# Kernel tuning notes

Hardware: AMD Instinct MI355X
Metric: run time of the kernel (lower is better)

Reference implementation:

```python
import jax, jax.numpy as jnp
import numpy as np


def _conv1x1(x, W, b):
    # 1x1 conv == per-pixel channel matmul: x [B,C,H,W], W [O,C], b [O]
    return jnp.einsum('bchw,oc->bohw', x, W) + b[None, :, None, None]


def setup_inputs() -> dict:
    key = jax.random.key(0)
    ks = jax.random.split(key, 9)
    B, C, H, W = 16, 512, 32, 32
    s = 1.0 / np.sqrt(C)
    inp = {
        'x': jax.random.normal(ks[0], (B, C, H, W), dtype=jnp.float32),
        'Wq': jax.random.normal(ks[1], (C, C), dtype=jnp.float32) * s,
        'bq': jax.random.normal(ks[2], (C,), dtype=jnp.float32) * 0.01,
        'Wk': jax.random.normal(ks[3], (C, C), dtype=jnp.float32) * s,
        'bk': jax.random.normal(ks[4], (C,), dtype=jnp.float32) * 0.01,
        'Wv': jax.random.normal(ks[5], (C, C), dtype=jnp.float32) * s,
        'bv': jax.random.normal(ks[6], (C,), dtype=jnp.float32) * 0.01,
        'Wo': jax.random.normal(ks[7], (C, C), dtype=jnp.float32) * s,
        'bo': jax.random.normal(ks[8], (C,), dtype=jnp.float32) * 0.01,
    }
    return inp


def reference(x, Wq, bq, Wk, bk, Wv, bv, Wo, bo):
    B, C, H, W = x.shape
    q = _conv1x1(x, Wq, bq)
    k = _conv1x1(x, Wk, bk)
    v = _conv1x1(x, Wv, bv)
    hw = H * W
    qf = q.reshape(B, C, hw)  # [B,C,HW]
    kf = k.reshape(B, C, hw)
    vf = v.reshape(B, C, hw)
    # scores[b,i,j] = sum_c q[b,c,i] * k[b,c,j], scaled by c^-0.5
    scores = jnp.einsum('bci,bcj->bij', qf, kf) * (C ** -0.5)
    attn = jax.nn.softmax(scores, axis=2)  # softmax over keys j
    # out[b,c,i] = sum_j v[b,c,j] * attn[b,i,j]
    out = jnp.einsum('bcj,bij->bci', vf, attn).reshape(B, C, H, W)
    out = _conv1x1(out, Wo, bo)
    return x + out
```

## Files before the change

kernel.cpp:

```cpp
#include <hip/hip_runtime.h>
#include <hip/hip_bf16.h>
#include <math.h>


typedef __bf16 bf16x8 __attribute__((ext_vector_type(8)));
typedef float  f32x16 __attribute__((ext_vector_type(16)));

__device__ __forceinline__ unsigned short f2bf(float f) {
    unsigned u = __float_as_uint(f);
    u += 0x7fff + ((u >> 16) & 1);
    return (unsigned short)(u >> 16);
}

__device__ __forceinline__ void gload_lds16(const void* g, void* l) {
    __builtin_amdgcn_global_load_lds(
        (const __attribute__((address_space(1))) void*)g,
        (__attribute__((address_space(3))) void*)l, 16, 0, 0);
}

struct GemmP {
    const unsigned short* A;
    const unsigned short* B;
    void* C;
    const float* bias;
    const float* resid;
    float* lsum;
    int M, N, K, ldA, ldB;
    long sA, sB, sC, sR;
    int ln_nn, ln_pb;
    float scale;
};

template<bool OUT_F32, int BIAS_MODE, bool RESID, int EXPM>
__device__ __forceinline__ void gemm_body(const GemmP p, int L,
                                          unsigned short* Als,
                                          unsigned short* Bls)
{
    const int xcd = L & 7;
    const int idx = L >> 3;
    const int bz  = xcd * 2 + (idx >> p.ln_pb);
    const int w   = idx & ((1 << p.ln_pb) - 1);
    const int m0  = (w >> p.ln_nn) << 7;
    const int n0  = (w & ((1 << p.ln_nn) - 1)) << 7;

    const unsigned short* A = p.A + bz * p.sA;
    const unsigned short* B = p.B + bz * p.sB;

    const int tid  = threadIdx.x;
    const int lane = tid & 63;
    const int wave = tid >> 6;
    const int wm   = wave >> 1;
    const int wn   = wave & 1;

    const int ar = lane >> 2;
    const int ak = (((lane & 3) ^ ((ar >> 1) & 3))) * 8;

    const unsigned short* agp = A + (long)(m0 + wave * 16 + ar) * p.ldA + ak;
    const unsigned short* bgp = B + (long)(n0 + wave * 16 + ar) * p.ldB + ak;
    const long aj = 64L * p.ldA;
    const long bj = 64L * p.ldB;

    unsigned short* alw  = Als + wave * 512;
    unsigned short* alwh = Als + (wave + 4) * 512;
    unsigned short* blw  = Bls + wave * 512;
    unsigned short* blwh = Bls + (wave + 4) * 512;

    const int ln31 = lane & 31;
    const int hi   = lane >> 5;
    const int swz  = ((ln31 >> 1) & 3) << 3;
    const int aoff = (wm * 64 + ln31) * 32;
    const int boff = (wn * 64 + ln31) * 32;
    const int koff0 = (hi * 8) ^ swz;
    const int koff1 = (16 + hi * 8) ^ swz;

    f32x16 acc[2][2] = {};

    const int nsteps = p.K >> 5;

    auto STAGE = [&](int sel) {
        gload_lds16(agp,      alw  + sel * 4096);
        gload_lds16(agp + aj, alwh + sel * 4096);
        gload_lds16(bgp,      blw  + sel * 4096);
        gload_lds16(bgp + bj, blwh + sel * 4096);
        agp += 32; bgp += 32;
    };

    auto COMPUTE = [&](int sel) {
        const unsigned short* Ap = Als + sel * 4096;
        const unsigned short* Bp = Bls + sel * 4096;
        bf16x8 af[2][2], bfr[2][2];
        #pragma unroll
        for (int mt = 0; mt < 2; ++mt) {
            af[mt][0] = *(const bf16x8*)&Ap[aoff + mt * 1024 + koff0];
            af[mt][1] = *(const bf16x8*)&Ap[aoff + mt * 1024 + koff1];
        }
        #pragma unroll
        for (int nt = 0; nt < 2; ++nt) {
            bfr[nt][0] = *(const bf16x8*)&Bp[boff + nt * 1024 + koff0];
            bfr[nt][1] = *(const bf16x8*)&Bp[boff + nt * 1024 + koff1];
        }
        #pragma unroll
        for (int ks = 0; ks < 2; ++ks)
            #pragma unroll
            for (int mt = 0; mt < 2; ++mt)
                #pragma unroll
                for (int nt = 0; nt < 2; ++nt)
                    acc[mt][nt] = __builtin_amdgcn_mfma_f32_32x32x16_bf16(
                        af[mt][ks], bfr[nt][ks], acc[mt][nt], 0, 0, 0);
    };

    STAGE(0);
    __syncthreads();

    for (int t = 0; t < nsteps; t += 2) {
        STAGE(1);
        COMPUTE(0);
        __syncthreads();
        if (t + 2 < nsteps) STAGE(0);
        COMPUTE(1);
        __syncthreads();
    }

    float* Cf = (float*)p.C + bz * p.sC;
    unsigned short* Ch = (unsigned short*)p.C + bz * p.sC;
    const float* resid = RESID ? (p.resid + bz * p.sR) : nullptr;
    const int N = p.N;

    if (EXPM == 1) {
        float* lrow = p.lsum + bz * (long)p.M;
        #pragma unroll
        for (int mt = 0; mt < 2; ++mt) {
            #pragma unroll
            for (int r = 0; r < 16; ++r) {
                const int row = m0 + wm * 64 + mt * 32 +
                                (r & 3) + 8 * (r >> 2) + 4 * hi;
                float rs = 0.0f;
                #pragma unroll
                for (int nt = 0; nt < 2; ++nt) {
                    const int col = n0 + wn * 64 + nt * 32 + ln31;
                    const float e = __expf(acc[mt][nt][r] * p.scale);
                    rs += e;
                    Ch[(long)row * N + col] = f2bf(e);
                }
                rs += __shfl_xor(rs, 1);
                rs += __shfl_xor(rs, 2);
                rs += __shfl_xor(rs, 4);
                rs += __shfl_xor(rs, 8);
                rs += __shfl_xor(rs, 16);
                if (ln31 == 0) atomicAdd(&lrow[row], rs);
            }
        }
    } else {
        #pragma unroll
        for (int mt = 0; mt < 2; ++mt) {
            float linv[16];
            if (EXPM == 2) {
                const float* lrow = p.lsum + bz * (long)p.M;
                #pragma unroll
                for (int r = 0; r < 16; ++r)
                    linv[r] = 1.0f / lrow[m0 + wm * 64 + mt * 32 +
                                          (r & 3) + 8 * (r >> 2) + 4 * hi];
            }
            #pragma unroll
            for (int nt = 0; nt < 2; ++nt) {
                const int col = n0 + wn * 64 + nt * 32 + ln31;
                const float bn = (BIAS_MODE == 2) ? p.bias[col] : 0.0f;
                #pragma unroll
                for (int r = 0; r < 16; ++r) {
                    const int row = m0 + wm * 64 + mt * 32 +
                                    (r & 3) + 8 * (r >> 2) + 4 * hi;
                    float val = acc[mt][nt][r] + bn;
                    if (BIAS_MODE == 1) val += p.bias[row];
                    if (EXPM == 2) val *= linv[r];
                    const long o = (long)row * N + col;
                    if (RESID) val += resid[o];
                    if (OUT_F32) Cf[o] = val;
                    else         Ch[o] = f2bf(val);
                }
            }
        }
    }
}

template<bool OUT_F32, int BIAS_MODE, bool RESID, int EXPM>
__global__ __launch_bounds__(256) void gemm_bt_mfma(GemmP p)
{
    __shared__ unsigned short Als[2 * 4096];
    __shared__ unsigned short Bls[2 * 4096];
    gemm_body<OUT_F32, BIAS_MODE, RESID, EXPM>(p, blockIdx.x, Als, Bls);
}

__global__ __launch_bounds__(256) void gemm_qkv_fused(GemmP pqk, GemmP pv, int split)
{
    __shared__ unsigned short Als[2 * 4096];
    __shared__ unsigned short Bls[2 * 4096];
    if ((int)blockIdx.x < split)
        gemm_body<false, 2, false, 0>(pqk, blockIdx.x, Als, Bls);
    else
        gemm_body<false, 1, false, 0>(pv, blockIdx.x - split, Als, Bls);
}

__global__ __launch_bounds__(256) void prep_all(
    const float* __restrict__ x, unsigned short* __restrict__ xT,
    const float* __restrict__ Wq, const float* __restrict__ Wk,
    const float* __restrict__ Wv, const float* __restrict__ Wo,
    const float* __restrict__ bq, const float* __restrict__ bk,
    unsigned short* __restrict__ Wb, float* __restrict__ biasqk,
    float* __restrict__ lsum)
{
    const int b = blockIdx.x;
    const int t = threadIdx.x;
    if (b < 8192) {
        __shared__ float tl[32][33];
        const int batch = b >> 9;
        const int rem = b & 511;
        const int p0 = (rem & 31) * 32;
        const int c0 = (rem >> 5) * 32;
        const float* xb = x + (long)batch * 524288;
        unsigned short* xTb = xT + (long)batch * 524288;
        const int tx = t & 31;
        const int ty = t >> 5;
        #pragma unroll
        for (int i = 0; i < 4; ++i)
            tl[ty + 8 * i][tx] = xb[(long)(c0 + ty + 8 * i) * 1024 + p0 + tx];
        __syncthreads();
        #pragma unroll
        for (int i = 0; i < 4; ++i)
            xTb[(long)(p0 + ty + 8 * i) * 512 + c0 + tx] = f2bf(tl[tx][ty + 8 * i]);
    } else if (b < 9216) {
        const int wb = b - 8192;
        const float* srcs[4] = {Wq, Wk, Wv, Wo};
        const float* s = srcs[wb >> 8];
        unsigned short* d = Wb + (long)(wb >> 8) * 262144;
        const int i = ((wb & 255) * 256 + t) * 4;
        const float4 f = *(const float4*)(s + i);
        ushort4 h;
        h.x = f2bf(f.x); h.y = f2bf(f.y); h.z = f2bf(f.z); h.w = f2bf(f.w);
        *(ushort4*)(d + i) = h;
    } else {
        biasqk[t]       = bq[t];
        biasqk[256 + t] = bq[256 + t];
        biasqk[512 + t] = bk[t];
        biasqk[768 + t] = bk[256 + t];
        #pragma unroll
        for (int i = 0; i < 64; ++i) lsum[i * 256 + t] = 0.0f;
    }
}

extern "C" void kernel_launch(void* const* d_in, const int* in_sizes, int n_in,
                              void* d_out, int out_size, void* d_ws, size_t ws_size,
                              hipStream_t stream)
{
    const float* x  = (const float*)d_in[0];
    const float* Wq = (const float*)d_in[1];
    const float* bq = (const float*)d_in[2];
    const float* Wk = (const float*)d_in[3];
    const float* bk = (const float*)d_in[4];
    const float* Wv = (const float*)d_in[5];
    const float* bv = (const float*)d_in[6];
    const float* Wo = (const float*)d_in[7];
    const float* bo = (const float*)d_in[8];
    float* out = (float*)d_out;

    const int Bn = 16, C = 512, HW = 1024;
    const long CHW = (long)C * HW;
    const long SHW = (long)HW * HW;

    unsigned short* xT   = (unsigned short*)d_ws;
    unsigned short* qkT  = xT + Bn * CHW;
    unsigned short* vB   = qkT + Bn * SHW;
    unsigned short* expS = vB + Bn * CHW;
    unsigned short* Wb   = expS + Bn * SHW;
    float* biasqk = (float*)(Wb + 4 * 262144);
    float* lsum   = biasqk + 1024;
    unsigned short* OT = xT;

    unsigned short* Wvb = Wb + 2 * 262144;
    unsigned short* Wob = Wb + 3 * 262144;

    const dim3 blk(256);
    const float scale = 0.044194173824159216f;

    prep_all<<<dim3(9217), blk, 0, stream>>>(x, xT, Wq, Wk, Wv, Wo, bq, bk,
                                             Wb, biasqk, lsum);

    GemmP pqk = { xT, Wb, qkT, biasqk, nullptr, nullptr,
                  HW, 2 * C, C, C, C, CHW, 0, SHW, 0, 3, 6, 0.0f };
    GemmP pv  = { Wvb, xT, vB, bv, nullptr, nullptr,
                  C, HW, C, C, C, 0, CHW, CHW, 0, 3, 5, 0.0f };
    gemm_qkv_fused<<<dim3(1536), blk, 0, stream>>>(pqk, pv, 1024);

    GemmP ps  = { qkT, qkT + C, expS, nullptr, nullptr, lsum,
                  HW, HW, C, 2 * C, 2 * C, SHW, SHW, SHW, 0, 3, 6, scale };
    gemm_bt_mfma<false, 0, false, 1><<<dim3(1024), blk, 0, stream>>>(ps);

    GemmP po  = { expS, vB, OT, nullptr, nullptr, lsum,
                  HW, C, HW, HW, HW, SHW, CHW, CHW, 0, 2, 5, 0.0f };
    gemm_bt_mfma<false, 0, false, 2><<<dim3(512), blk, 0, stream>>>(po);

    GemmP pout = { Wob, OT, out, bo, x, nullptr,
                   C, HW, C, C, C, 0, CHW, CHW, CHW, 3, 5, 0.0f };
    gemm_bt_mfma<true, 1, true, 0><<<dim3(512), blk, 0, stream>>>(pout);
}
```

Before: 241.3 us.

## Switch GEMM mainloop to triple-buffered LDS pipeline with one barrier per step

Replaces the double-buffered K loop, which has two __syncthreads per pair of steps, with a three-stage LDS ring. Each step has one barrier gated by a partial vmcnt wait, so two global-to-LDS loads stay in flight while the MFMAs run on the current buffer. The aim is to hide global load latency and halve barrier count. LDS use per block goes from 32 KB to 48 KB, which may lower occupancy, and the explicit waitcnt/sched_barrier sequencing is fragile.

```diff
diff --git a/kernel.cpp b/kernel.cpp
--- a/kernel.cpp
+++ b/kernel.cpp
@@ -60,11 +60,6 @@
     const long aj = 64L * p.ldA;
     const long bj = 64L * p.ldB;
 
-    unsigned short* alw  = Als + wave * 512;
-    unsigned short* alwh = Als + (wave + 4) * 512;
-    unsigned short* blw  = Bls + wave * 512;
-    unsigned short* blwh = Bls + (wave + 4) * 512;
-
     const int ln31 = lane & 31;
     const int hi   = lane >> 5;
     const int swz  = ((ln31 >> 1) & 3) << 3;
@@ -78,10 +73,12 @@
     const int nsteps = p.K >> 5;
 
     auto STAGE = [&](int sel) {
-        gload_lds16(agp,      alw  + sel * 4096);
-        gload_lds16(agp + aj, alwh + sel * 4096);
-        gload_lds16(bgp,      blw  + sel * 4096);
-        gload_lds16(bgp + bj, blwh + sel * 4096);
+        unsigned short* a0 = Als + sel * 4096;
+        unsigned short* b0 = Bls + sel * 4096;
+        gload_lds16(agp,      a0 + wave * 512);
+        gload_lds16(agp + aj, a0 + (wave + 4) * 512);
+        gload_lds16(bgp,      b0 + wave * 512);
+        gload_lds16(bgp + bj, b0 + (wave + 4) * 512);
         agp += 32; bgp += 32;
     };
 
@@ -110,16 +107,25 @@
     };
 
     STAGE(0);
-    __syncthreads();
-
-    for (int t = 0; t < nsteps; t += 2) {
-        STAGE(1);
-        COMPUTE(0);
-        __syncthreads();
-        if (t + 2 < nsteps) STAGE(0);
-        COMPUTE(1);
-        __syncthreads();
+    STAGE(1);
+
+    int bc = 0, bn = 1, bs = 2;
+    for (int t = 0; t < nsteps - 1; ++t) {
+        __builtin_amdgcn_sched_barrier(0);
+        asm volatile("s_waitcnt vmcnt(4)" ::: "memory");
+        __builtin_amdgcn_s_barrier();
+        asm volatile("" ::: "memory");
+        __builtin_amdgcn_sched_barrier(0);
+        if (t + 2 < nsteps) STAGE(bs);
+        COMPUTE(bc);
+        const int tmp = bc; bc = bn; bn = bs; bs = tmp;
     }
+    __builtin_amdgcn_sched_barrier(0);
+    asm volatile("s_waitcnt vmcnt(0)" ::: "memory");
+    __builtin_amdgcn_s_barrier();
+    asm volatile("" ::: "memory");
+    __builtin_amdgcn_sched_barrier(0);
+    COMPUTE(bc);
 
     float* Cf = (float*)p.C + bz * p.sC;
     unsigned short* Ch = (unsigned short*)p.C + bz * p.sC;
@@ -164,12 +170,12 @@
             #pragma unroll
             for (int nt = 0; nt < 2; ++nt) {
                 const int col = n0 + wn * 64 + nt * 32 + ln31;
-                const float bn = (BIAS_MODE == 2) ? p.bias[col] : 0.0f;
+                const float bn2 = (BIAS_MODE == 2) ? p.bias[col] : 0.0f;
                 #pragma unroll
                 for (int r = 0; r < 16; ++r) {
                     const int row = m0 + wm * 64 + mt * 32 +
                                     (r & 3) + 8 * (r >> 2) + 4 * hi;
-                    float val = acc[mt][nt][r] + bn;
+                    float val = acc[mt][nt][r] + bn2;
                     if (BIAS_MODE == 1) val += p.bias[row];
                     if (EXPM == 2) val *= linv[r];
                     const long o = (long)row * N + col;
@@ -185,15 +191,15 @@
 template<bool OUT_F32, int BIAS_MODE, bool RESID, int EXPM>
 __global__ __launch_bounds__(256) void gemm_bt_mfma(GemmP p)
 {
-    __shared__ unsigned short Als[2 * 4096];
-    __shared__ unsigned short Bls[2 * 4096];
+    __shared__ unsigned short Als[3 * 4096];
+    __shared__ unsigned short Bls[3 * 4096];
     gemm_body<OUT_F32, BIAS_MODE, RESID, EXPM>(p, blockIdx.x, Als, Bls);
 }
 
 __global__ __launch_bounds__(256) void gemm_qkv_fused(GemmP pqk, GemmP pv, int split)
 {
-    __shared__ unsigned short Als[2 * 4096];
-    __shared__ unsigned short Bls[2 * 4096];
+    __shared__ unsigned short Als[3 * 4096];
+    __shared__ unsigned short Bls[3 * 4096];
     if ((int)blockIdx.x < split)
         gemm_body<false, 2, false, 0>(pqk, blockIdx.x, Als, Bls);
     else
```

Result: faster. 233.9 us (-3.1%).
